# Performance work log

Measured on AMD Instinct MI355X. Metric: run time of the kernel, lower is better.

Reference implementation:

```python
import jax, jax.numpy as jnp
import numpy as np

N = 20000      # nodes
E = 320000     # edges (avg degree 16)
IN = 128       # in_size
H = 256        # layer_size
DEPTH = 2      # extra hidden layers
BN_EPS = 1e-5


def setup_inputs() -> dict:
    key = jax.random.key(0)
    ks = jax.random.split(key, 16)
    x = jax.random.normal(ks[0], (N, IN), jnp.float32)
    edge_index = jax.random.randint(ks[1], (2, E), 0, N)
    # first MLP layer: Linear(2*IN -> H) + BatchNorm1d(H) (inference stats)
    W0 = jax.random.normal(ks[2], (H, 2 * IN), jnp.float32) * 0.05
    b0 = jnp.zeros((H,), jnp.float32)
    g0 = jnp.ones((H,), jnp.float32)
    beta0 = jnp.zeros((H,), jnp.float32)
    m0 = jax.random.normal(ks[3], (H,), jnp.float32) * 0.1
    v0 = jax.random.uniform(ks[4], (H,), jnp.float32, 0.5, 1.5)
    # DEPTH repeated layers: Linear(H -> H) + BatchNorm1d(H)
    Ws = jax.random.normal(ks[5], (DEPTH, H, H), jnp.float32) * 0.05
    bs = jnp.zeros((DEPTH, H), jnp.float32)
    gs = jnp.ones((DEPTH, H), jnp.float32)
    betas = jnp.zeros((DEPTH, H), jnp.float32)
    ms = jax.random.normal(ks[6], (DEPTH, H), jnp.float32) * 0.1
    vs = jax.random.uniform(ks[7], (DEPTH, H), jnp.float32, 0.5, 1.5)
    return {"x": x, "edge_index": edge_index,
            "W0": W0, "b0": b0, "g0": g0, "beta0": beta0, "m0": m0, "v0": v0,
            "Ws": Ws, "bs": bs, "gs": gs, "betas": betas, "ms": ms, "vs": vs}


def _bn(h, g, b, m, v):
    # BatchNorm1d in inference mode (running stats)
    return (h - m) * (g * jax.lax.rsqrt(v + BN_EPS)) + b


def reference(x, edge_index, W0, b0, g0, beta0, m0, v0, Ws, bs, gs, betas, ms, vs):
    src = edge_index[0]  # x_j (source / neighbor)
    dst = edge_index[1]  # x_i (target), also scatter index
    # gather + concat: [E, 2*IN]
    h = jnp.concatenate([x[dst], x[src]], axis=-1)
    # edge MLP (dropout is identity in eval mode)
    h = jax.nn.selu(_bn(h @ W0.T + b0, g0, beta0, m0, v0))
    for i in range(DEPTH):
        h = jax.nn.selu(_bn(h @ Ws[i].T + bs[i], gs[i], betas[i], ms[i], vs[i]))
    # scatter-mean aggregation onto target nodes
    agg_sum = jax.ops.segment_sum(h, dst, num_segments=N)
    cnt = jax.ops.segment_sum(jnp.ones((E,), h.dtype), dst, num_segments=N)
    agg = agg_sum / jnp.maximum(cnt, 1.0)[:, None]
    return (agg, h)  # (aggregated node features, edge activations)
```

## Files before the change

kernel.cpp:

```cpp
#include <hip/hip_runtime.h>
#include <hip/hip_bf16.h>

#define IN_F 128
#define HF 256
#define BN_EPS 1e-5f
#define SELU_SCALE 1.0507009873554805f
#define SELU_ALPHA 1.6732632423543772f

typedef __attribute__((ext_vector_type(8))) _Float16 half8;
typedef __attribute__((ext_vector_type(2))) unsigned int u32x2;
typedef __attribute__((ext_vector_type(4))) float f32x4;

__device__ __forceinline__ short f2h(float f) {
    _Float16 h = (_Float16)f;
    return __builtin_bit_cast(short, h);
}

__device__ __forceinline__ float selu_f(float x) {
    const float SA = SELU_SCALE * SELU_ALPHA;
    float e = __expf(x);
    return x > 0.f ? SELU_SCALE * x : SA * e - SA;
}

__device__ __forceinline__ unsigned int pk2h(float a, float b) {
    return __builtin_bit_cast(unsigned int, __builtin_amdgcn_cvt_pkrtz(a, b));
}

__device__ __forceinline__ void gld_lds16(const void* g, void* l) {
    __builtin_amdgcn_global_load_lds(
        (const __attribute__((address_space(1))) unsigned int*)g,
        (__attribute__((address_space(3))) unsigned int*)l, 16, 0, 0);
}

__global__ void prep_kernel(const float* __restrict__ W0, const float* __restrict__ b0,
                            const float* __restrict__ g0, const float* __restrict__ beta0,
                            const float* __restrict__ m0, const float* __restrict__ v0,
                            const float* __restrict__ Ws, const float* __restrict__ bs,
                            const float* __restrict__ gs, const float* __restrict__ betas,
                            const float* __restrict__ ms, const float* __restrict__ vs,
                            unsigned short* __restrict__ Wf, float* __restrict__ biasArr) {
    int b = blockIdx.x;
    int layer = b >> 8;
    int n = b & 255;
    int k = threadIdx.x;
    const float *W, *bb, *g, *be, *m, *v;
    if (layer == 0) { W = W0; bb = b0; g = g0; be = beta0; m = m0; v = v0; }
    else {
        int i = layer - 1;
        W = Ws + (size_t)i * HF * HF; bb = bs + i * HF; g = gs + i * HF;
        be = betas + i * HF; m = ms + i * HF; v = vs + i * HF;
    }
    float s = g[n] * rsqrtf(v[n] + BN_EPS);
    int kk = k >> 5, kc = (k >> 3) & 3, j = k & 7;
    Wf[((((size_t)layer * 8 + kk) * 4 + kc) * 256 + n) * 8 + j] =
        (unsigned short)f2h(W[n * HF + k] * s);
    if (k == 0) biasArr[layer * HF + n] = (bb[n] - m[n]) * s + be[n];
}

__global__ void count_kernel(const int* __restrict__ dstI, int* __restrict__ cnt, int E) {
    int i = blockIdx.x * 256 + threadIdx.x;
    if (i < E) atomicAdd(cnt + dstI[i], 1);
}

__global__ void scan_kernel(const int* __restrict__ cnt, int* __restrict__ wrk, int n) {
    __shared__ int s[1024];
    __shared__ int carryS;
    int t = threadIdx.x;
    if (t == 0) carryS = 0;
    __syncthreads();
    for (int c0 = 0; c0 < n; c0 += 1024) {
        int i = c0 + t;
        int v = (i < n) ? cnt[i] : 0;
        s[t] = v;
        __syncthreads();
#pragma unroll
        for (int d = 1; d < 1024; d <<= 1) {
            int add = (t >= d) ? s[t - d] : 0;
            __syncthreads();
            s[t] += add;
            __syncthreads();
        }
        int incl = s[t];
        int base = carryS;
        if (i < n) wrk[i] = base + incl - v;
        __syncthreads();
        if (t == 1023) carryS = base + s[1023];
        __syncthreads();
    }
}

__global__ void scatter_kernel(const int* __restrict__ dstI, int* __restrict__ wrk,
                               int* __restrict__ perm, int E) {
    int i = blockIdx.x * 256 + threadIdx.x;
    if (i < E) {
        int p = atomicAdd(wrk + dstI[i], 1);
        perm[p] = i;
    }
}

__global__ void finalize_kernel(float* __restrict__ agg, const int* __restrict__ cnt) {
    int n = blockIdx.x;
    float c = fmaxf((float)cnt[n], 1.f);
    agg[(size_t)n * HF + threadIdx.x] = agg[(size_t)n * HF + threadIdx.x] / c;
}

__global__ __launch_bounds__(256, 3)
void fused_kernel(const float* __restrict__ x,
                  const int* __restrict__ dstI, const int* __restrict__ srcI,
                  const int* __restrict__ perm,
                  const unsigned char* __restrict__ Wfb,
                  const float* __restrict__ biasArr,
                  unsigned char* __restrict__ hB, float* __restrict__ agg) {
    __shared__ __align__(16) unsigned char lds[49152];
    __shared__ int peL[64];
    __shared__ int pdL[64];

    const int base = blockIdx.x * 64;
    const int t = threadIdx.x;
    const int lane = t & 63;
    const int w = t >> 6;
    const int lrow = lane & 15;
    const int lgrp = lane >> 4;

    auto stageB = [&](int L, int kk) {
        const unsigned char* src = Wfb + ((size_t)(L * 8 + kk) << 14);
        unsigned char* dstBase = lds + 32768 + w * 1024;
#pragma unroll
        for (int i = 0; i < 4; ++i)
            gld_lds16(src + (i * 256 + t) * 16, dstBase + i * 4096);
    };

    stageB(0, 0);

    {
        int r = t >> 2, q = t & 3;
        int e = perm[base + r];
        int idx = (q < 2 ? dstI : srcI)[e];
        const float* xr = x + (size_t)idx * IN_F + (q & 1) * 64;
        int swz = (r & 7) << 4;
#pragma unroll
        for (int u = 0; u < 16; ++u) {
            f32x4 v = *(const f32x4*)(xr + u * 4);
            u32x2 hv = {pk2h(v[0], v[1]), pk2h(v[2], v[3])};
            *(u32x2*)&lds[r * 512 + ((q * 128 + u * 8) ^ swz)] = hv;
        }
    }

    f32x4 acc[4][4];
    const f32x4 zero = {0.f, 0.f, 0.f, 0.f};

#pragma unroll
    for (int L = 0; L < 3; ++L) {
#pragma unroll
        for (int mi = 0; mi < 4; ++mi)
#pragma unroll
            for (int ni = 0; ni < 4; ++ni) acc[mi][ni] = zero;

#pragma unroll
        for (int kk = 0; kk < 8; ++kk) {
            __syncthreads();

            half8 af[4], bf[4];
#pragma unroll
            for (int mi = 0; mi < 4; ++mi) {
                int row = mi * 16 + lrow;
                af[mi] = *(const half8*)&lds[row * 512 +
                    ((kk * 64 + lgrp * 16) ^ ((row & 7) << 4))];
            }
#pragma unroll
            for (int ni = 0; ni < 4; ++ni)
                bf[ni] = *(const half8*)&lds[32768 + lgrp * 4096 +
                                             (w * 64 + ni * 16 + lrow) * 16];
            __syncthreads();

            if (kk < 7) stageB(L, kk + 1);
            else if (L < 2) stageB(L + 1, 0);

            if (L < 2) {
#pragma unroll
                for (int mi = 0; mi < 4; ++mi)
#pragma unroll
                    for (int ni = 0; ni < 4; ++ni)
                        acc[mi][ni] = __builtin_amdgcn_mfma_f32_16x16x32_f16(
                            bf[ni], af[mi], acc[mi][ni], 0, 0, 0);
            } else {
#pragma unroll
                for (int mi = 0; mi < 4; ++mi)
#pragma unroll
                    for (int ni = 0; ni < 4; ++ni)
                        acc[mi][ni] = __builtin_amdgcn_mfma_f32_16x16x32_f16(
                            af[mi], bf[ni], acc[mi][ni], 0, 0, 0);
            }
        }

        if (L < 2) {
#pragma unroll
            for (int ni = 0; ni < 4; ++ni) {
                f32x4 bv = *(const f32x4*)(biasArr + L * HF + w * 64 + ni * 16 + lgrp * 4);
#pragma unroll
                for (int mi = 0; mi < 4; ++mi) {
                    int row = mi * 16 + lrow;
                    float v0 = selu_f(acc[mi][ni][0] + bv[0]);
                    float v1 = selu_f(acc[mi][ni][1] + bv[1]);
                    float v2 = selu_f(acc[mi][ni][2] + bv[2]);
                    float v3 = selu_f(acc[mi][ni][3] + bv[3]);
                    u32x2 d = {pk2h(v0, v1), pk2h(v2, v3)};
                    *(u32x2*)&lds[row * 512 +
                        ((w * 128 + ni * 32 + lgrp * 8) ^ ((row & 7) << 4))] = d;
                }
            }
        } else {
            if (t < 64) {
                int e = perm[base + t];
                peL[t] = e;
                pdL[t] = dstI[e];
            }
            float bc[4];
#pragma unroll
            for (int ni = 0; ni < 4; ++ni) bc[ni] = biasArr[2 * HF + w * 64 + ni * 16 + lrow];
            unsigned char* EP = lds + 32768;
            int curD = -1;
            float carry = 0.f;
#pragma unroll
            for (int cc = 0; cc < 4; ++cc) {
                if (cc) __syncthreads();
#pragma unroll
                for (int ni = 0; ni < 4; ++ni)
#pragma unroll
                    for (int r = 0; r < 4; ++r) {
                        int er = lgrp * 4 + r;
                        int cg = w * 64 + ni * 16 + lrow;
                        float val = selu_f(acc[cc][ni][r] + bc[ni]);
                        *(float*)&EP[er * 1024 + ((cg * 4) ^ ((er & 7) << 4))] = val;
                    }
                __syncthreads();
#pragma unroll
                for (int i = 0; i < 4; ++i) {
                    int f = t + i * 256;
                    int row = f >> 6, ch = f & 63;
                    f32x4 v = *(const f32x4*)&EP[row * 1024 + ((ch * 16) ^ ((row & 7) << 4))];
                    *(f32x4*)(hB + (size_t)peL[cc * 16 + row] * 1024 + ch * 16) = v;
                }
#pragma unroll
                for (int r = 0; r < 16; ++r) {
                    float v = *(const float*)&EP[r * 1024 + ((t * 4) ^ ((r & 7) << 4))];
                    int d = pdL[cc * 16 + r];
                    if (d != curD) {
                        if (curD >= 0) atomicAdd(agg + (size_t)curD * HF + t, carry);
                        carry = 0.f;
                        curD = d;
                    }
                    carry += v;
                }
            }
            atomicAdd(agg + (size_t)curD * HF + t, carry);
        }
    }
}

extern "C" void kernel_launch(void* const* d_in, const int* in_sizes, int n_in,
                              void* d_out, int out_size, void* d_ws, size_t ws_size,
                              hipStream_t stream) {
    const float* x     = (const float*)d_in[0];
    const int*   ei    = (const int*)d_in[1];
    const float* W0    = (const float*)d_in[2];
    const float* b0    = (const float*)d_in[3];
    const float* g0    = (const float*)d_in[4];
    const float* beta0 = (const float*)d_in[5];
    const float* m0    = (const float*)d_in[6];
    const float* v0    = (const float*)d_in[7];
    const float* Ws    = (const float*)d_in[8];
    const float* bs    = (const float*)d_in[9];
    const float* gs    = (const float*)d_in[10];
    const float* betas = (const float*)d_in[11];
    const float* ms    = (const float*)d_in[12];
    const float* vs    = (const float*)d_in[13];

    const int Nn = in_sizes[0] / IN_F;
    const int E  = in_sizes[1] / 2;

    float* agg  = (float*)d_out;
    float* hptr = agg + (size_t)Nn * HF;

    char* wsb = (char*)d_ws;
    unsigned short* Wf = (unsigned short*)wsb;
    float* biasArr = (float*)(wsb + 393216);
    int* cnt  = (int*)(wsb + 396288);
    int* wrk  = (int*)(wsb + 476288);
    int* perm = (int*)(wsb + 556288);

    const int* srcI = ei;
    const int* dstI = ei + E;

    prep_kernel<<<3 * HF, HF, 0, stream>>>(W0, b0, g0, beta0, m0, v0,
                                           Ws, bs, gs, betas, ms, vs, Wf, biasArr);
    hipMemsetAsync(cnt, 0, (size_t)Nn * sizeof(int), stream);
    hipMemsetAsync(agg, 0, (size_t)Nn * HF * sizeof(float), stream);
    count_kernel<<<(E + 255) / 256, 256, 0, stream>>>(dstI, cnt, E);
    scan_kernel<<<1, 1024, 0, stream>>>(cnt, wrk, Nn);
    scatter_kernel<<<(E + 255) / 256, 256, 0, stream>>>(dstI, wrk, perm, E);

    fused_kernel<<<E / 64, 256, 0, stream>>>(x, dstI, srcI, perm,
                                             (const unsigned char*)Wf, biasArr,
                                             (unsigned char*)hptr, agg);

    finalize_kernel<<<Nn, HF, 0, stream>>>(agg, cnt);
}
```

Before: 320.8 us.

## Parallelize prefix scan across blocks and write final-layer output directly from registers

Replaces the single-block serial-chunk scan with a three-kernel block-parallel scan (local scan, serial tops, add), using the agg buffer as scratch for block totals before it is zeroed. The last layer now uses the same MFMA operand order as the earlier layers, applies bias+SELU in registers, writes h rows to global memory directly from accumulators, and stages only 32 rows at a time in LDS for the column-wise segmented reduction. This halves the LDS staging passes and removes the LDS round-trip for the h store. The trade-offs are two extra kernel launches and scattered 16-byte global stores in place of coalesced full-row stores.

Result: no change. 316.9 us (-1.2%).

```diff
diff --git a/kernel.cpp b/kernel.cpp
--- a/kernel.cpp
+++ b/kernel.cpp
@@ -62,31 +62,32 @@
     if (i < E) atomicAdd(cnt + dstI[i], 1);
 }
 
-__global__ void scan_kernel(const int* __restrict__ cnt, int* __restrict__ wrk, int n) {
+__global__ void scan_local(const int* __restrict__ cnt, int* __restrict__ wrk,
+                           int* __restrict__ btot, int n) {
     __shared__ int s[1024];
-    __shared__ int carryS;
-    int t = threadIdx.x;
-    if (t == 0) carryS = 0;
+    int b = blockIdx.x, t = threadIdx.x, i = b * 1024 + t;
+    int v = (i < n) ? cnt[i] : 0;
+    s[t] = v;
     __syncthreads();
-    for (int c0 = 0; c0 < n; c0 += 1024) {
-        int i = c0 + t;
-        int v = (i < n) ? cnt[i] : 0;
-        s[t] = v;
+#pragma unroll
+    for (int d = 1; d < 1024; d <<= 1) {
+        int add = (t >= d) ? s[t - d] : 0;
         __syncthreads();
-#pragma unroll
-        for (int d = 1; d < 1024; d <<= 1) {
-            int add = (t >= d) ? s[t - d] : 0;
-            __syncthreads();
-            s[t] += add;
-            __syncthreads();
-        }
-        int incl = s[t];
-        int base = carryS;
-        if (i < n) wrk[i] = base + incl - v;
+        s[t] += add;
         __syncthreads();
-        if (t == 1023) carryS = base + s[1023];
-        __syncthreads();
-    }
+    }
+    if (i < n) wrk[i] = s[t] - v;
+    if (t == 1023) btot[b] = s[1023];
+}
+__global__ void scan_tops(int* __restrict__ btot, int nb) {
+    if (threadIdx.x == 0) {
+        int run = 0;
+        for (int i = 0; i < nb; ++i) { int v = btot[i]; btot[i] = run; run += v; }
+    }
+}
+__global__ void scan_add(int* __restrict__ wrk, const int* __restrict__ btot, int n) {
+    int i = blockIdx.x * 1024 + threadIdx.x;
+    if (i < n) wrk[i] += btot[blockIdx.x];
 }
 
 __global__ void scatter_kernel(const int* __restrict__ dstI, int* __restrict__ wrk,
@@ -176,21 +177,12 @@
             if (kk < 7) stageB(L, kk + 1);
             else if (L < 2) stageB(L + 1, 0);
 
-            if (L < 2) {
-#pragma unroll
-                for (int mi = 0; mi < 4; ++mi)
-#pragma unroll
-                    for (int ni = 0; ni < 4; ++ni)
-                        acc[mi][ni] = __builtin_amdgcn_mfma_f32_16x16x32_f16(
-                            bf[ni], af[mi], acc[mi][ni], 0, 0, 0);
-            } else {
-#pragma unroll
-                for (int mi = 0; mi < 4; ++mi)
-#pragma unroll
-                    for (int ni = 0; ni < 4; ++ni)
-                        acc[mi][ni] = __builtin_amdgcn_mfma_f32_16x16x32_f16(
-                            af[mi], bf[ni], acc[mi][ni], 0, 0, 0);
-            }
+#pragma unroll
+            for (int mi = 0; mi < 4; ++mi)
+#pragma unroll
+                for (int ni = 0; ni < 4; ++ni)
+                    acc[mi][ni] = __builtin_amdgcn_mfma_f32_16x16x32_f16(
+                        bf[ni], af[mi], acc[mi][ni], 0, 0, 0);
         }
 
         if (L < 2) {
@@ -210,41 +202,53 @@
                 }
             }
         } else {
+#pragma unroll
+            for (int ni = 0; ni < 4; ++ni) {
+                f32x4 bv = *(const f32x4*)(biasArr + 2 * HF + w * 64 + ni * 16 + lgrp * 4);
+#pragma unroll
+                for (int mi = 0; mi < 4; ++mi) {
+#pragma unroll
+                    for (int r = 0; r < 4; ++r)
+                        acc[mi][ni][r] = selu_f(acc[mi][ni][r] + bv[r]);
+                }
+            }
             if (t < 64) {
                 int e = perm[base + t];
                 peL[t] = e;
                 pdL[t] = dstI[e];
             }
-            float bc[4];
-#pragma unroll
-            for (int ni = 0; ni < 4; ++ni) bc[ni] = biasArr[2 * HF + w * 64 + ni * 16 + lrow];
-            unsigned char* EP = lds + 32768;
             int curD = -1;
             float carry = 0.f;
 #pragma unroll
-            for (int cc = 0; cc < 4; ++cc) {
-                if (cc) __syncthreads();
-#pragma unroll
-                for (int ni = 0; ni < 4; ++ni)
-#pragma unroll
-                    for (int r = 0; r < 4; ++r) {
-                        int er = lgrp * 4 + r;
-                        int cg = w * 64 + ni * 16 + lrow;
-                        float val = selu_f(acc[cc][ni][r] + bc[ni]);
-                        *(float*)&EP[er * 1024 + ((cg * 4) ^ ((er & 7) << 4))] = val;
-                    }
+            for (int p = 0; p < 2; ++p) {
+                if (p) __syncthreads();
+#pragma unroll
+                for (int m2 = 0; m2 < 2; ++m2) {
+                    int mi = p * 2 + m2;
+#pragma unroll
+                    for (int ni = 0; ni < 4; ++ni)
+#pragma unroll
+                        for (int r = 0; r < 4; ++r) {
+                            int er = m2 * 16 + lrow;
+                            int cg = w * 64 + ni * 16 + lgrp * 4 + r;
+                            *(float*)&lds[er * 1024 + ((cg * 4) ^ ((er & 7) << 4))] =
+                                acc[mi][ni][r];
+                        }
+                }
                 __syncthreads();
 #pragma unroll
-                for (int i = 0; i < 4; ++i) {
-                    int f = t + i * 256;
-                    int row = f >> 6, ch = f & 63;
-                    f32x4 v = *(const f32x4*)&EP[row * 1024 + ((ch * 16) ^ ((row & 7) << 4))];
-                    *(f32x4*)(hB + (size_t)peL[cc * 16 + row] * 1024 + ch * 16) = v;
-                }
-#pragma unroll
-                for (int r = 0; r < 16; ++r) {
-                    float v = *(const float*)&EP[r * 1024 + ((t * 4) ^ ((r & 7) << 4))];
-                    int d = pdL[cc * 16 + r];
+                for (int m2 = 0; m2 < 2; ++m2) {
+                    int mi = p * 2 + m2;
+                    size_t eoff = (size_t)peL[mi * 16 + lrow] << 10;
+#pragma unroll
+                    for (int ni = 0; ni < 4; ++ni)
+                        *(f32x4*)(hB + eoff + (w * 64 + ni * 16 + lgrp * 4) * 4) =
+                            acc[mi][ni];
+                }
+#pragma unroll
+                for (int r = 0; r < 32; ++r) {
+                    float v = *(const float*)&lds[r * 1024 + ((t * 4) ^ ((r & 7) << 4))];
+                    int d = pdL[p * 32 + r];
                     if (d != curD) {
                         if (curD >= 0) atomicAdd(agg + (size_t)curD * HF + t, carry);
                         carry = 0.f;
@@ -288,16 +292,21 @@
     int* cnt  = (int*)(wsb + 396288);
     int* wrk  = (int*)(wsb + 476288);
     int* perm = (int*)(wsb + 556288);
+    int* btot = (int*)agg;
 
     const int* srcI = ei;
     const int* dstI = ei + E;
+
+    const int nScan = (Nn + 1023) / 1024;
 
     prep_kernel<<<3 * HF, HF, 0, stream>>>(W0, b0, g0, beta0, m0, v0,
                                            Ws, bs, gs, betas, ms, vs, Wf, biasArr);
     hipMemsetAsync(cnt, 0, (size_t)Nn * sizeof(int), stream);
+    count_kernel<<<(E + 255) / 256, 256, 0, stream>>>(dstI, cnt, E);
+    scan_local<<<nScan, 1024, 0, stream>>>(cnt, wrk, btot, Nn);
+    scan_tops<<<1, 64, 0, stream>>>(btot, nScan);
+    scan_add<<<nScan, 1024, 0, stream>>>(wrk, btot, Nn);
     hipMemsetAsync(agg, 0, (size_t)Nn * HF * sizeof(float), stream);
-    count_kernel<<<(E + 255) / 256, 256, 0, stream>>>(dstI, cnt, E);
-    scan_kernel<<<1, 1024, 0, stream>>>(cnt, wrk, Nn);
     scatter_kernel<<<(E + 255) / 256, 256, 0, stream>>>(dstI, wrk, perm, E);
 
     fused_kernel<<<E / 64, 256, 0, stream>>>(x, dstI, srcI, perm,
```
